# Kernel tuning notes

Measured on AMD Instinct MI355X. Metric: run time of the kernel, lower is better.

The kernel has to match this reference:

```python
import jax, jax.numpy as jnp
import numpy as np

BIT_W = 8   # config.bit_wt
BIT_A = 8   # config.bit_act (activations sliced 2 bits at a time)
STRIDE = (1, 1)
PAD = 1


def _conv(a, w):
    # NCHW input, OIHW weight, stride 1, symmetric padding 1 (matches wrapped Conv2d)
    return jax.lax.conv_general_dilated(
        a, w, window_strides=STRIDE, padding=[(PAD, PAD), (PAD, PAD)],
        dimension_numbers=("NCHW", "OIHW", "NCHW"))


def setup_inputs() -> dict:
    key = jax.random.key(0)
    k1, k2, k3 = jax.random.split(key, 3)
    x = jax.random.normal(k1, (64, 64, 56, 56), dtype=jnp.float32)
    weight = jax.random.normal(k2, (64, 64, 3, 3), dtype=jnp.float32)
    bias = jax.random.normal(k3, (64,), dtype=jnp.float32)
    scale_a = jnp.full((1,), 20.0, dtype=jnp.float32)      # conv_q.scale
    scale_w = jnp.full((1,), 20.0, dtype=jnp.float32)      # wrapped_module.weight_scale
    zero_point = jnp.full((1,), -128.0, dtype=jnp.float32)  # conv_q.zero_point
    return {"x": x, "weight": weight, "bias": bias,
            "scale_a": scale_a, "scale_w": scale_w, "zero_point": zero_point}


def reference(x, weight, bias, scale_a, scale_w, zero_point):
    sa = scale_a[0]
    sw = scale_w[0]
    zp = zero_point[0]
    # activation quantization: round(x*scale_a - zero_point), clamp to [0, 2^bit_act - 1]
    q_in = jnp.clip(jnp.round(x * sa - zp), 0.0, 2.0 ** BIT_A - 1.0)
    # weight quantization: round(w * scale_w), interpreted in two's complement
    q_w = jnp.round(weight * sw)
    w_off = q_w + 2.0 ** BIT_W  # (w + (1 << bit_weight)) before bit masking

    acc = jnp.zeros((), dtype=jnp.float32)
    for ba in range(BIT_A // 2):
        # 2-bit activation slice: (a >> 2*ba) & 3
        a_sl = jnp.mod(jnp.floor(q_in / (4.0 ** ba)), 4.0)
        for bw in range(BIT_W):
            # weight bit bw: ((w + 2^B) >> bw) & 1
            w_bit = jnp.mod(jnp.floor(w_off / (2.0 ** bw)), 2.0)
            r = _conv(a_sl, w_bit)
            sgn = -1.0 if bw == BIT_W - 1 else 1.0  # MSB = sign bit (two's complement)
            acc = acc + sgn * (2.0 ** (2 * ba + bw)) * r

    # zero-point correction: conv(ones * zp, q_w) added back (no-op when zp == 0)
    acc = acc + zp * _conv(jnp.ones_like(q_in), q_w)

    out = acc / (sw * sa) + bias[None, :, None, None]
    return out
```

## Files before the change

### kernel.cpp

```cpp
#include <hip/hip_runtime.h>


typedef int v4i __attribute__((ext_vector_type(4)));

#define ROWB 80

__global__ __launch_bounds__(64) void prep_wq(const float* __restrict__ wt,
                                              const float* __restrict__ sw_p,
                                              const float* __restrict__ zp_p,
                                              signed char* __restrict__ w8,
                                              float* __restrict__ corr_tab) {
  const int o = blockIdx.x;
  const int i = threadIdx.x;
  const float sw = sw_p[0];
  const float* wp = wt + (size_t)(o * 64 + i) * 9;
  int q[9];
#pragma unroll
  for (int k = 0; k < 9; ++k) q[k] = (int)rintf(wp[k] * sw);
#pragma unroll
  for (int k = 0; k < 9; ++k)
    w8[(o * 9 + k) * 64 + i] = (signed char)(q[k] & 255);

  int stc[9], srw[9];
#pragma unroll
  for (int k = 0; k < 9; ++k) {
    int a = (int)(signed char)(q[k] & 255);
    int b = q[k];
#pragma unroll
    for (int off = 32; off; off >>= 1) {
      a += __shfl_xor(a, off);
      b += __shfl_xor(b, off);
    }
    stc[k] = a; srw[k] = b;
  }
  const float zp = zp_p[0];
  if (i < 9) {
    const int v = i / 3, hc = i % 3;
    float corr = 0.0f;
#pragma unroll
    for (int k = 0; k < 9; ++k) {
      const int kh = k / 3, kw = k % 3;
      const bool drop = (v == 1 && kh == 0) || (v == 2 && kh == 2) ||
                        (hc == 1 && kw == 0) || (hc == 2 && kw == 2);
      if (!drop) corr += 128.0f * (float)stc[k] + zp * (float)srw[k];
    }
    corr_tab[i * 64 + o] = corr;
  }
}

__global__ __launch_bounds__(256, 4) void conv_fused(
    const float* __restrict__ x, const signed char* __restrict__ w8,
    const float* __restrict__ corr_tab, const float* __restrict__ bias,
    const float* __restrict__ sa_p, const float* __restrict__ sw_p,
    const float* __restrict__ zp_p, float* __restrict__ out) {
  __shared__ __align__(16) signed char lds[6 * 58 * ROWB];
  const int tid = threadIdx.x;
  const int n = blockIdx.y;
  const int h0 = blockIdx.x * 4;
  const float sa = sa_p[0], zp = zp_p[0];
  const float* xim = x + (size_t)n * 200704;

#pragma unroll 2
  for (int it = 0; it < 6; ++it) {
    const int idx = tid + 256 * it;
    if (idx < 1344) {
      const int cg = idx & 15;
      const int rem = idx >> 4;
      const int row = (rem * 2341) >> 15;
      const int w4 = rem - row * 14;
      const int ih = h0 - 1 + row;
      const bool valid = (unsigned)ih < 56u;
      int* const dst = (int*)lds + (row * 58 + w4 * 4 + 1) * (ROWB / 4) + cg;
      if (valid) {
        float4 v[4];
#pragma unroll
        for (int j = 0; j < 4; ++j)
          v[j] = *(const float4*)(xim + (size_t)(cg * 4 + j) * 3136 + ih * 56 + w4 * 4);
#pragma unroll
        for (int e = 0; e < 4; ++e) {
          int dw = 0;
#pragma unroll
          for (int j = 0; j < 4; ++j) {
            const float xv = (&v[j].x)[e];
            float tq;
            {
#pragma clang fp contract(off)
              tq = xv * sa - zp;
            }
            float qf = rintf(tq);
            qf = fminf(fmaxf(qf, 0.0f), 255.0f);
            const int b = ((int)qf - 128) & 255;
            dw |= b << (8 * j);
          }
          dst[e * (ROWB / 4)] = dw;
        }
      } else {
#pragma unroll
        for (int e = 0; e < 4; ++e) dst[e * (ROWB / 4)] = 0;
      }
    } else {
      const int z = idx - 1344;
      const int loc = z >> 4, d = z & 15;
      const int row = loc >> 1, side = loc & 1;
      ((int*)lds)[(row * 58 + side * 57) * (ROWB / 4) + d] = 0;
    }
  }
  __syncthreads();

  const int lane = tid & 63;
  const int wv = tid >> 6;
  const int phalf = wv & 1;
  const int ogp = wv >> 1;
  const int ln = lane & 15;
  const int kg = lane >> 4;
  const int oa = ogp * 32 + ln;

  const signed char* wba = w8 + (size_t)oa * 576 + kg * 16;
  v4i Ba[9], Bb[9];
#pragma unroll
  for (int t = 0; t < 9; ++t) {
    Ba[t] = *(const v4i*)(wba + t * 64);
    Bb[t] = *(const v4i*)(wba + 9216 + t * 64);
  }

  const float sw = sw_p[0];
  const float rden = 1.0f / (sw * sa);
  const float boa = bias[oa], bob = bias[oa + 16];
  const float cFa = corr_tab[oa];
  const float cFb = corr_tab[oa + 16];
  float* const outa = out + (size_t)(n * 64 + oa) * 3136 + h0 * 56;
  float* const outb = outa + 16 * 3136;

#pragma unroll 1
  for (int t = 0; t < 7; ++t) {
    const int pb = phalf * 112 + t * 16;
    const int pa = pb + ln;
    const int hr = (pa * 9363) >> 19;
    const int wc = pa - hr * 56;
    const signed char* ab = lds + (hr * 58 + wc) * ROWB + kg * 16;
    v4i acca = {0, 0, 0, 0}, accb = {0, 0, 0, 0};
#pragma unroll
    for (int kh = 0; kh < 3; ++kh) {
#pragma unroll
      for (int kw = 0; kw < 3; ++kw) {
        const v4i A = *(const v4i*)(ab + (kh * 58 + kw) * ROWB);
        acca = __builtin_amdgcn_mfma_i32_16x16x64_i8(A, Ba[kh * 3 + kw], acca, 0, 0, 0);
        accb = __builtin_amdgcn_mfma_i32_16x16x64_i8(A, Bb[kh * 3 + kw], accb, 0, 0, 0);
      }
    }
    const int pxb = pb + kg * 4;
    float ta[4], tb[4];
#pragma unroll
    for (int e = 0; e < 4; ++e) {
      const int px = pxb + e;
      const int hh = (px * 9363) >> 19;
      const int ww = px - hh * 56;
      const int hg = h0 + hh;
      float ca = cFa, cb = cFb;
      if ((hg == 0) | (hg == 55) | (ww == 0) | (ww == 55)) {
        const int vcase = (hg == 0) ? 1 : ((hg == 55) ? 2 : 0);
        const int hcase = (ww == 0) ? 1 : ((ww == 55) ? 2 : 0);
        const int cidx = (vcase * 3 + hcase) * 64;
        ca = corr_tab[cidx + oa];
        cb = corr_tab[cidx + oa + 16];
      }
      ta[e] = ((float)acca[e] + ca) * rden + boa;
      tb[e] = ((float)accb[e] + cb) * rden + bob;
    }
    *(float4*)(outa + pxb) = make_float4(ta[0], ta[1], ta[2], ta[3]);
    *(float4*)(outb + pxb) = make_float4(tb[0], tb[1], tb[2], tb[3]);
  }
}

extern "C" void kernel_launch(void* const* d_in, const int* in_sizes, int n_in,
                              void* d_out, int out_size, void* d_ws, size_t ws_size,
                              hipStream_t stream) {
  const float* x    = (const float*)d_in[0];
  const float* wt   = (const float*)d_in[1];
  const float* bias = (const float*)d_in[2];
  const float* sa   = (const float*)d_in[3];
  const float* sw   = (const float*)d_in[4];
  const float* zp   = (const float*)d_in[5];
  float* out = (float*)d_out;

  char* ws = (char*)d_ws;
  signed char* w8 = (signed char*)ws;
  float* corr_tab = (float*)(ws + 36864);

  prep_wq<<<64, 64, 0, stream>>>(wt, sw, zp, w8, corr_tab);
  conv_fused<<<dim3(14, 64), 256, 0, stream>>>(x, w8, corr_tab, bias, sa, sw, zp, out);
}
```

Measured before the change: 125.4 us.

## Swizzle block order, use packed u8 convert, nontemporal output stores

The 2D grid is flattened to 896 blocks and remapped so consecutive blocks are spread across XCD-style groups of 8. Activation quantization now packs four bytes with v_cvt_pk_u8_f32 inline asm, which saturates to 0..255, and an XOR with 0x80 replaces the explicit clamp, subtract and shift/or sequence. Output stores become nontemporal, and the staging loop unroll goes from 2 to 3. These target instruction count in the quantize stage and cache pollution from streaming writes. The risk is that inline asm rounding and saturation semantics must match the original clamp exactly.

```diff
diff --git a/kernel.cpp b/kernel.cpp
--- a/kernel.cpp
+++ b/kernel.cpp
@@ -2,6 +2,7 @@
 
 
 typedef int v4i __attribute__((ext_vector_type(4)));
+typedef float v4f __attribute__((ext_vector_type(4)));
 
 #define ROWB 80
 
@@ -55,12 +56,14 @@
     const float* __restrict__ zp_p, float* __restrict__ out) {
   __shared__ __align__(16) signed char lds[6 * 58 * ROWB];
   const int tid = threadIdx.x;
-  const int n = blockIdx.y;
-  const int h0 = blockIdx.x * 4;
+  const int b = blockIdx.x;
+  const int g = (b & 7) * 112 + (b >> 3);
+  const int n = (g * 2341) >> 15;
+  const int h0 = (g - n * 14) * 4;
   const float sa = sa_p[0], zp = zp_p[0];
   const float* xim = x + (size_t)n * 200704;
 
-#pragma unroll 2
+#pragma unroll 3
   for (int it = 0; it < 6; ++it) {
     const int idx = tid + 256 * it;
     if (idx < 1344) {
@@ -72,27 +75,28 @@
       const bool valid = (unsigned)ih < 56u;
       int* const dst = (int*)lds + (row * 58 + w4 * 4 + 1) * (ROWB / 4) + cg;
       if (valid) {
-        float4 v[4];
+        v4f v[4];
 #pragma unroll
         for (int j = 0; j < 4; ++j)
-          v[j] = *(const float4*)(xim + (size_t)(cg * 4 + j) * 3136 + ih * 56 + w4 * 4);
+          v[j] = *(const v4f*)(xim + (size_t)(cg * 4 + j) * 3136 + ih * 56 + w4 * 4);
 #pragma unroll
         for (int e = 0; e < 4; ++e) {
-          int dw = 0;
+          float qf[4];
 #pragma unroll
           for (int j = 0; j < 4; ++j) {
-            const float xv = (&v[j].x)[e];
             float tq;
             {
 #pragma clang fp contract(off)
-              tq = xv * sa - zp;
+              tq = v[j][e] * sa - zp;
             }
-            float qf = rintf(tq);
-            qf = fminf(fmaxf(qf, 0.0f), 255.0f);
-            const int b = ((int)qf - 128) & 255;
-            dw |= b << (8 * j);
+            qf[j] = rintf(tq);
           }
-          dst[e * (ROWB / 4)] = dw;
+          unsigned dw;
+          asm("v_cvt_pk_u8_f32 %0, %1, 0, %2" : "=v"(dw) : "v"(qf[0]), "v"(0u));
+          asm("v_cvt_pk_u8_f32 %0, %1, 1, %2" : "=v"(dw) : "v"(qf[1]), "v"(dw));
+          asm("v_cvt_pk_u8_f32 %0, %1, 2, %2" : "=v"(dw) : "v"(qf[2]), "v"(dw));
+          asm("v_cvt_pk_u8_f32 %0, %1, 3, %2" : "=v"(dw) : "v"(qf[3]), "v"(dw));
+          dst[e * (ROWB / 4)] = (int)(dw ^ 0x80808080u);
         }
       } else {
 #pragma unroll
@@ -167,8 +171,10 @@
       ta[e] = ((float)acca[e] + ca) * rden + boa;
       tb[e] = ((float)accb[e] + cb) * rden + bob;
     }
-    *(float4*)(outa + pxb) = make_float4(ta[0], ta[1], ta[2], ta[3]);
-    *(float4*)(outb + pxb) = make_float4(tb[0], tb[1], tb[2], tb[3]);
+    const v4f va = {ta[0], ta[1], ta[2], ta[3]};
+    const v4f vb = {tb[0], tb[1], tb[2], tb[3]};
+    __builtin_nontemporal_store(va, (v4f*)(outa + pxb));
+    __builtin_nontemporal_store(vb, (v4f*)(outb + pxb));
   }
 }
 
@@ -188,5 +194,5 @@
   float* corr_tab = (float*)(ws + 36864);
 
   prep_wq<<<64, 64, 0, stream>>>(wt, sw, zp, w8, corr_tab);
-  conv_fused<<<dim3(14, 64), 256, 0, stream>>>(x, w8, corr_tab, bias, sa, sw, zp, out);
+  conv_fused<<<896, 256, 0, stream>>>(x, w8, corr_tab, bias, sa, sw, zp, out);
 }
```

Result: slower. 136.6 us (+9.0%).
